# Optimization experiments

Hardware: AMD Instinct MI355X
Metric: run time of the kernel (lower is better)

## Reference

```python
import jax, jax.numpy as jnp
import numpy as np

K_TOP = 2  # n_experts_per_tok
W_SCALE = 0.02  # keep activations numerically tame


def setup_inputs() -> dict:
    key = jax.random.key(0)
    ks = jax.random.split(key, 8)
    D, F, E = 1024, 1024, 8
    B, T = 4, 2048
    x = jax.random.normal(ks[0], (B, T, D), dtype=jnp.float32)
    router_w = jax.random.normal(ks[1], (D, E), dtype=jnp.float32) * W_SCALE
    sg = jax.random.normal(ks[2], (D, F), dtype=jnp.float32) * W_SCALE
    su = jax.random.normal(ks[3], (D, F), dtype=jnp.float32) * W_SCALE
    sd = jax.random.normal(ks[4], (F, D), dtype=jnp.float32) * W_SCALE
    wg = jax.random.normal(ks[5], (E, D, F), dtype=jnp.float32) * W_SCALE
    wu = jax.random.normal(ks[6], (E, D, F), dtype=jnp.float32) * W_SCALE
    wd = jax.random.normal(ks[7], (E, F, D), dtype=jnp.float32) * W_SCALE
    return {"x": x, "router_w": router_w, "sg": sg, "su": su, "sd": sd,
            "wg": wg, "wu": wu, "wd": wd}


def reference(x, router_w, sg, su, sd, wg, wu, wd):
    B, T, D = x.shape
    E = wg.shape[0]
    flat = x.reshape(-1, D)                       # [N, D]
    N = flat.shape[0]

    # shared SwiGLU expert (n_shared_experts = 1)
    shared = (jax.nn.silu(flat @ sg) * (flat @ su)) @ sd  # [N, D]

    # top-k softmax router with renormalization
    probs = jax.nn.softmax(flat @ router_w, axis=-1)      # [N, E]
    topk_p, topk_i = jax.lax.top_k(probs, K_TOP)          # [N, K]
    topk_p = topk_p / (jnp.sum(topk_p, axis=-1, keepdims=True) + 1e-9)

    # dense combine weights: scatter renormalized probs into [N, E]
    cw = jnp.zeros((N, E), dtype=flat.dtype).at[
        jnp.arange(N)[:, None], topk_i].add(topk_p)

    # per-expert SwiGLU on all tokens, weighted combine (jit-friendly MoE form)
    h = jax.nn.silu(jnp.einsum('nd,edf->nef', flat, wg)) \
        * jnp.einsum('nd,edf->nef', flat, wu)             # [N, E, F]
    eo = jnp.einsum('nef,efd->ned', h, wd)                # [N, E, D]
    routed = jnp.einsum('ned,ne->nd', eo, cw)             # [N, D]

    return (shared + routed).reshape(B, T, D)
```

## Files before the change

kernel.cpp:

```cpp
#include <hip/hip_runtime.h>

#define N_TOK    8192
#define D_DIM    1024
#define F_DIM    1024
#define NESH     9
#define MAX_RTD  18432
#define MAX_ROWS 26624
#define BM 256
#define NK 16

#define MO 16
#define MT 25

typedef float  f4    __attribute__((ext_vector_type(4)));
typedef float  f32x4 __attribute__((ext_vector_type(4)));
typedef short  s16x8 __attribute__((ext_vector_type(8)));
typedef unsigned short u16x8 __attribute__((ext_vector_type(8)));
typedef unsigned short u16x4 __attribute__((ext_vector_type(4)));

static __device__ __forceinline__ unsigned short f2bf(float f) {
    union { float f; unsigned u; } v; v.f = f;
    unsigned r = v.u + 0x7FFFu + ((v.u >> 16) & 1u);
    return (unsigned short)(r >> 16);
}
static __device__ __forceinline__ float bf2f(unsigned short u) {
    union { unsigned u; float f; } v; v.u = ((unsigned)u) << 16; return v.f;
}

#define GLDS(gp, lp) __builtin_amdgcn_global_load_lds( \
    (const __attribute__((address_space(1))) void*)(gp), \
    (__attribute__((address_space(3))) void*)(lp), 16, 0, 0)

__global__ __launch_bounds__(256) void k_transpose(
    const float* __restrict__ wg, const float* __restrict__ wu,
    const float* __restrict__ wd, const float* __restrict__ sg,
    const float* __restrict__ su, const float* __restrict__ sd,
    unsigned short* __restrict__ wgt, unsigned short* __restrict__ wut,
    unsigned short* __restrict__ wdt)
{
    int bx = blockIdx.x;
    int m = bx >> 8;
    int tile = bx & 255;
    int ty = tile >> 4, tx = tile & 15;
    int set = m / 9, e = m % 9;
    const float* src; unsigned short* dst;
    if (set == 0)      { src = (e < 8) ? wg + (size_t)e*1048576 : sg; dst = wgt + (size_t)e*1048576; }
    else if (set == 1) { src = (e < 8) ? wu + (size_t)e*1048576 : su; dst = wut + (size_t)e*1048576; }
    else               { src = (e < 8) ? wd + (size_t)e*1048576 : sd; dst = wdt + (size_t)e*1048576; }

    __shared__ unsigned short ts[64 * 67];
    int t = threadIdx.x;
    int rT0 = ty * 64, cT0 = tx * 64;
    #pragma unroll
    for (int i = 0; i < 4; i++) {
        int idx = t + i * 256;
        int a  = idx >> 4;
        int b4 = (idx & 15) * 4;
        f4 v = *(const f4*)(src + (size_t)(cT0 + a) * 1024 + rT0 + b4);
        ts[a * 67 + b4 + 0] = f2bf(v[0]);
        ts[a * 67 + b4 + 1] = f2bf(v[1]);
        ts[a * 67 + b4 + 2] = f2bf(v[2]);
        ts[a * 67 + b4 + 3] = f2bf(v[3]);
    }
    __syncthreads();
    #pragma unroll
    for (int i = 0; i < 2; i++) {
        int slot = t + i * 256;
        int r  = slot >> 3;
        int c8 = (slot & 7) * 8;
        u16x8 o;
        #pragma unroll
        for (int k = 0; k < 8; k++) o[k] = ts[(c8 + k) * 67 + r];
        *(u16x8*)&dst[(size_t)(rT0 + r) * 1024 + cT0 + c8] = o;
    }
}

__global__ __launch_bounds__(256) void k_router(
    const float* __restrict__ x, const float* __restrict__ rw,
    unsigned short* __restrict__ xb,
    int* __restrict__ tk_i, float* __restrict__ tk_w)
{
    int wid = threadIdx.x >> 6, lane = threadIdx.x & 63;
    int n = blockIdx.x * 4 + wid;
    const float* xr = x + (size_t)n * D_DIM;
    unsigned short* xbr = xb + (size_t)n * D_DIM;
    float acc[8] = {0,0,0,0,0,0,0,0};
    #pragma unroll
    for (int it = 0; it < 4; it++) {
        int d0 = it * 256 + lane * 4;
        f4 xv = *(const f4*)(xr + d0);
        #pragma unroll
        for (int j = 0; j < 4; j++) {
            f4 r0 = *(const f4*)(rw + (size_t)(d0 + j) * 8);
            f4 r1 = *(const f4*)(rw + (size_t)(d0 + j) * 8 + 4);
            acc[0] += xv[j]*r0[0]; acc[1] += xv[j]*r0[1]; acc[2] += xv[j]*r0[2]; acc[3] += xv[j]*r0[3];
            acc[4] += xv[j]*r1[0]; acc[5] += xv[j]*r1[1]; acc[6] += xv[j]*r1[2]; acc[7] += xv[j]*r1[3];
        }
        u16x4 o; o[0]=f2bf(xv[0]); o[1]=f2bf(xv[1]); o[2]=f2bf(xv[2]); o[3]=f2bf(xv[3]);
        *(u16x4*)&xbr[d0] = o;
    }
    #pragma unroll
    for (int e = 0; e < 8; e++)
        for (int off = 32; off; off >>= 1)
            acc[e] += __shfl_xor(acc[e], off, 64);
    if (lane == 0) {
        float mx = acc[0];
        for (int e = 1; e < 8; e++) mx = fmaxf(mx, acc[e]);
        float p[8], s = 0.f;
        for (int e = 0; e < 8; e++) { p[e] = expf(acc[e] - mx); s += p[e]; }
        int i0 = 0;
        for (int e = 1; e < 8; e++) if (p[e] > p[i0]) i0 = e;
        int i1 = (i0 == 0) ? 1 : 0;
        for (int e = 0; e < 8; e++) if (e != i0 && p[e] > p[i1]) i1 = e;
        float p0 = p[i0] / s, p1 = p[i1] / s;
        float rs = p0 + p1 + 1e-9f;
        tk_i[2*n] = i0;  tk_i[2*n+1] = i1;
        tk_w[2*n] = p0 / rs;  tk_w[2*n+1] = p1 / rs;
    }
}

__global__ __launch_bounds__(1024) void k_count_scatter(
    const int* __restrict__ tk_i, const float* __restrict__ tk_w,
    int* __restrict__ meta,
    int* __restrict__ row_token, int* __restrict__ row_expert,
    int* __restrict__ tok_pos)
{
    __shared__ int cnt[1024 * 9];
    __shared__ int tot[8];
    __shared__ int off[9];
    const int t = threadIdx.x;
    const int lane = t & 63;
    const int wid = t >> 6;

    #pragma unroll
    for (int e = 0; e < 8; e++) cnt[t * 9 + e] = 0;
    __syncthreads();

    #pragma unroll
    for (int j = 0; j < 8; j++) {
        int n = t * 8 + j;
        cnt[t * 9 + tk_i[2 * n]]++;
        cnt[t * 9 + tk_i[2 * n + 1]]++;
    }
    __syncthreads();

    if (wid < 8) {
        const int e = wid;
        int carry = 0;
        for (int c = 0; c < 16; c++) {
            int i = c * 64 + lane;
            int v = cnt[i * 9 + e];
            int s = v;
            #pragma unroll
            for (int d = 1; d < 64; d <<= 1) {
                int u = __shfl_up(s, d, 64);
                if (lane >= d) s += u;
            }
            cnt[i * 9 + e] = s - v + carry;
            carry += __shfl(s, 63, 64);
        }
        if (lane == 0) tot[e] = carry;
    }
    __syncthreads();

    if (t == 0) {
        int acc = 0;
        #pragma unroll
        for (int e = 0; e < 8; e++) {
            off[e] = acc;
            meta[MO + e] = acc;
            acc += ((tot[e] + 255) >> 8) << 8;
        }
        off[8] = acc;
        meta[MO + 8] = acc;
        meta[MT] = acc + N_TOK;
    }
    __syncthreads();

    #pragma unroll
    for (int j = 0; j < 8; j++) {
        int n = t * 8 + j;
        #pragma unroll
        for (int k = 0; k < 2; k++) {
            int e = tk_i[2 * n + k];
            int pos = off[e] + cnt[t * 9 + e];
            cnt[t * 9 + e] = cnt[t * 9 + e] + 1;
            row_token[pos] = n; row_expert[pos] = e;
            tok_pos[2 * n + k] = pos;
        }
        int ps = off[8] + n;
        row_token[ps] = n; row_expert[ps] = 8;
    }
    #pragma unroll
    for (int e = 0; e < 8; e++) {
        int start = off[e] + tot[e], end = off[e + 1];
        for (int i = start + t; i < end; i += 1024) row_token[i] = -1;
    }
}

__global__ __launch_bounds__(512, 2) void k_gemm1(
    const unsigned short* __restrict__ xb,
    const unsigned short* __restrict__ wgt,
    const unsigned short* __restrict__ wut,
    const int* __restrict__ row_token,
    const int* __restrict__ row_expert,
    const int* __restrict__ meta,
    unsigned short* __restrict__ h)
{
    const int total = meta[MT];
    const int orig = blockIdx.x;
    const int bid = (orig & 7) * 104 + (orig >> 3);
    const int rt = bid >> 3, ct = bid & 7;
    const int row0 = rt * BM;
    if (row0 >= total) return;
    const int e = row_expert[row0];

    __shared__ __align__(16) unsigned short sA[4 * 256 * 32];
    __shared__ __align__(16) unsigned short sBg[4 * 128 * 32];
    __shared__ __align__(16) unsigned short sBu[4 * 128 * 32];

    const int t = threadIdx.x;
    const int lane = t & 63;
    const int klane = lane >> 4;
    const int wid = t >> 6;
    const int wr = wid >> 2, wc = wid & 3;

    const unsigned short* aA[2];
    #pragma unroll
    for (int r = 0; r < 2; r++) {
        int slot = t + r * 512;
        int row = slot >> 2;
        int cg = (slot & 3) ^ ((row >> 1) & 3);
        int tok = row_token[row0 + row];
        if (tok < 0) tok = 0;
        aA[r] = xb + (size_t)tok * D_DIM + cg * 8;
    }
    const int brow = t >> 2;
    const int bcg = (t & 3) ^ ((brow >> 1) & 3);
    const unsigned short* bG = wgt + ((size_t)e * F_DIM + ct * 128 + brow) * D_DIM + bcg * 8;
    const unsigned short* bU = wut + ((size_t)e * F_DIM + ct * 128 + brow) * D_DIM + bcg * 8;

#define ST_A(sl, ko) do { \
    GLDS(aA[0] + (ko), &sA[(sl) * 8192 + t * 8]); \
    GLDS(aA[1] + (ko), &sA[(sl) * 8192 + (t + 512) * 8]); } while (0)
#define ST_G(sl, ko) GLDS(bG + (ko), &sBg[(sl) * 4096 + t * 8])
#define ST_U(sl, ko) GLDS(bU + (ko), &sBu[(sl) * 4096 + t * 8])

#define G1_PHASE(bb, ss, hh, STAGE_STMT, VM_STMT) do { \
    const unsigned short* pA = &sA[((bb)*2 + (ss)) * 8192]; \
    const unsigned short* pG = &sBg[((bb)*2 + (ss)) * 4096]; \
    const unsigned short* pU = &sBu[((bb)*2 + (ss)) * 4096]; \
    s16x8 a_[4], g_[2], q_[2]; \
    _Pragma("unroll") \
    for (int mi = 0; mi < 4; mi++) { \
        int row = wr * 128 + (hh) * 64 + mi * 16 + (lane & 15); \
        a_[mi] = *(const s16x8*)&pA[row * 32 + ((klane ^ ((row >> 1) & 3)) << 3)]; } \
    _Pragma("unroll") \
    for (int ni = 0; ni < 2; ni++) { \
        int row = wc * 32 + ni * 16 + (lane & 15); \
        int ix = row * 32 + ((klane ^ ((row >> 1) & 3)) << 3); \
        g_[ni] = *(const s16x8*)&pG[ix]; \
        q_[ni] = *(const s16x8*)&pU[ix]; } \
    STAGE_STMT; \
    VM_STMT; \
    asm volatile("s_barrier" ::: "memory"); \
    __builtin_amdgcn_s_setprio(1); \
    _Pragma("unroll") \
    for (int mi = 0; mi < 4; mi++) \
        _Pragma("unroll") \
        for (int ni = 0; ni < 2; ni++) { \
            accg[(hh)*4+mi][ni] = __builtin_amdgcn_mfma_f32_16x16x32_bf16(a_[mi], g_[ni], accg[(hh)*4+mi][ni], 0, 0, 0); \
            accu[(hh)*4+mi][ni] = __builtin_amdgcn_mfma_f32_16x16x32_bf16(a_[mi], q_[ni], accu[(hh)*4+mi][ni], 0, 0, 0); } \
    __builtin_amdgcn_s_setprio(0); \
    asm volatile("s_barrier" ::: "memory"); \
} while (0)

    f32x4 accg[8][2] = {}, accu[8][2] = {};

    ST_A(0, 0);  ST_G(0, 0);  ST_U(0, 0);
    ST_A(1, 32); ST_G(1, 32); ST_U(1, 32);
    ST_A(2, 64); ST_G(2, 64); ST_U(2, 64);
    ST_A(3, 96);
    asm volatile("s_waitcnt vmcnt(6)" ::: "memory");
    asm volatile("s_barrier" ::: "memory");

    for (int u = 0; u < NK; u++) {
        const int b = u & 1, nb = b ^ 1;
        const int o1 = (u + 1) * 64 + 32, o2 = (u + 2) * 64;
        G1_PHASE(b, 0, 0, if (u < NK-1) { ST_G(nb*2+1, o1); ST_U(nb*2+1, o1); }, );
        G1_PHASE(b, 0, 1, if (u < NK-2) { ST_A(b*2, o2); }, );
        G1_PHASE(b, 1, 0, if (u < NK-2) { ST_G(b*2, o2); ST_U(b*2, o2); }, );
        G1_PHASE(b, 1, 1, if (u < NK-2) { ST_A(b*2+1, o2+32); },
                 if (u < NK-2) { asm volatile("s_waitcnt vmcnt(6)" ::: "memory"); }
                 else if (u == NK-2) { asm volatile("s_waitcnt vmcnt(0)" ::: "memory"); });
    }

    #pragma unroll
    for (int mf = 0; mf < 8; mf++)
        #pragma unroll
        for (int r = 0; r < 4; r++) {
            int grow = row0 + wr * 128 + mf * 16 + (lane >> 4) * 4 + r;
            unsigned short* hrow = h + (size_t)grow * F_DIM + ct * 128 + wc * 32 + (lane & 15);
            #pragma unroll
            for (int ni = 0; ni < 2; ni++) {
                float g = accg[mf][ni][r], uu = accu[mf][ni][r];
                float sv = g / (1.f + __expf(-g));
                hrow[ni * 16] = f2bf(sv * uu);
            }
        }
#undef ST_A
#undef ST_G
#undef ST_U
#undef G1_PHASE
}

__global__ __launch_bounds__(512, 2) void k_gemm2(
    const unsigned short* __restrict__ h,
    const unsigned short* __restrict__ wdt,
    const int* __restrict__ row_expert,
    const int* __restrict__ meta,
    unsigned short* __restrict__ eo,
    float* __restrict__ out)
{
    const int total = meta[MT];
    const int off8 = meta[MO + 8];
    const int orig = blockIdx.x;
    const int bid = (orig & 7) * 52 + (orig >> 3);
    const int rt = bid >> 2, ct = bid & 3;
    const int row0 = rt * BM;
    if (row0 >= total) return;
    const int e = row_expert[row0];

    __shared__ __align__(16) unsigned short sA[4 * 256 * 32];
    __shared__ __align__(16) unsigned short sB[4 * 256 * 32];

    const int t = threadIdx.x;
    const int lane = t & 63;
    const int klane = lane >> 4;
    const int wid = t >> 6;
    const int wr = wid >> 2, wc = wid & 3;

    const unsigned short* aA[2];
    const unsigned short* bB[2];
    #pragma unroll
    for (int r = 0; r < 2; r++) {
        int slot = t + r * 512;
        int row = slot >> 2;
        int cg = (slot & 3) ^ ((row >> 1) & 3);
        aA[r] = h + (size_t)(row0 + row) * F_DIM + cg * 8;
        bB[r] = wdt + ((size_t)e * D_DIM + ct * 256 + row) * F_DIM + cg * 8;
    }

#define ST_A2(sl, ko) do { \
    GLDS(aA[0] + (ko), &sA[(sl) * 8192 + t * 8]); \
    GLDS(aA[1] + (ko), &sA[(sl) * 8192 + (t + 512) * 8]); } while (0)
#define ST_B2(sl, ko) do { \
    GLDS(bB[0] + (ko), &sB[(sl) * 8192 + t * 8]); \
    GLDS(bB[1] + (ko), &sB[(sl) * 8192 + (t + 512) * 8]); } while (0)

#define G2_PHASE(bb, ss, hh, STAGE_STMT, VM_STMT) do { \
    const unsigned short* pA = &sA[((bb)*2 + (ss)) * 8192]; \
    const unsigned short* pB = &sB[((bb)*2 + (ss)) * 8192]; \
    s16x8 a_[4], b_[4]; \
    _Pragma("unroll") \
    for (int mi = 0; mi < 4; mi++) { \
        int row = wr * 128 + (hh) * 64 + mi * 16 + (lane & 15); \
        a_[mi] = *(const s16x8*)&pA[row * 32 + ((klane ^ ((row >> 1) & 3)) << 3)]; } \
    _Pragma("unroll") \
    for (int ni = 0; ni < 4; ni++) { \
        int row = wc * 64 + ni * 16 + (lane & 15); \
        b_[ni] = *(const s16x8*)&pB[row * 32 + ((klane ^ ((row >> 1) & 3)) << 3)]; } \
    STAGE_STMT; \
    VM_STMT; \
    asm volatile("s_barrier" ::: "memory"); \
    __builtin_amdgcn_s_setprio(1); \
    _Pragma("unroll") \
    for (int mi = 0; mi < 4; mi++) \
        _Pragma("unroll") \
        for (int ni = 0; ni < 4; ni++) \
            acc[(hh)*4+mi][ni] = __builtin_amdgcn_mfma_f32_16x16x32_bf16(a_[mi], b_[ni], acc[(hh)*4+mi][ni], 0, 0, 0); \
    __builtin_amdgcn_s_setprio(0); \
    asm volatile("s_barrier" ::: "memory"); \
} while (0)

    f32x4 acc[8][4] = {};

    ST_A2(0, 0);  ST_B2(0, 0);
    ST_A2(1, 32); ST_B2(1, 32);
    ST_A2(2, 64); ST_B2(2, 64);
    ST_A2(3, 96);
    asm volatile("s_waitcnt vmcnt(6)" ::: "memory");
    asm volatile("s_barrier" ::: "memory");

    for (int u = 0; u < NK; u++) {
        const int b = u & 1, nb = b ^ 1;
        const int o1 = (u + 1) * 64 + 32, o2 = (u + 2) * 64;
        G2_PHASE(b, 0, 0, if (u < NK-1) { ST_B2(nb*2+1, o1); }, );
        G2_PHASE(b, 0, 1, if (u < NK-2) { ST_A2(b*2, o2); }, );
        G2_PHASE(b, 1, 0, if (u < NK-2) { ST_B2(b*2, o2); }, );
        G2_PHASE(b, 1, 1, if (u < NK-2) { ST_A2(b*2+1, o2+32); },
                 if (u < NK-2) { asm volatile("s_waitcnt vmcnt(6)" ::: "memory"); }
                 else if (u == NK-2) { asm volatile("s_waitcnt vmcnt(0)" ::: "memory"); });
    }

    if (e < 8) {
        #pragma unroll
        for (int mf = 0; mf < 8; mf++)
            #pragma unroll
            for (int r = 0; r < 4; r++) {
                int grow = row0 + wr * 128 + mf * 16 + (lane >> 4) * 4 + r;
                unsigned short* erow = eo + (size_t)grow * D_DIM + ct * 256 + wc * 64 + (lane & 15);
                #pragma unroll
                for (int ni = 0; ni < 4; ni++)
                    erow[ni * 16] = f2bf(acc[mf][ni][r]);
            }
    } else {
        #pragma unroll
        for (int mf = 0; mf < 8; mf++)
            #pragma unroll
            for (int r = 0; r < 4; r++) {
                int grow = row0 + wr * 128 + mf * 16 + (lane >> 4) * 4 + r;
                int tok = grow - off8;
                float* orow = out + (size_t)tok * D_DIM + ct * 256 + wc * 64 + (lane & 15);
                #pragma unroll
                for (int ni = 0; ni < 4; ni++)
                    orow[ni * 16] = acc[mf][ni][r];
            }
    }
#undef ST_A2
#undef ST_B2
#undef G2_PHASE
}

__global__ __launch_bounds__(256) void k_combine(
    const unsigned short* __restrict__ eo,
    const int* __restrict__ tok_pos, const float* __restrict__ tk_w,
    float* __restrict__ out)
{
    const int t = threadIdx.x;
    const int n = blockIdx.x * 2 + (t >> 7);
    const int c0 = (t & 127) * 8;
    const int p0 = tok_pos[2 * n], p1 = tok_pos[2 * n + 1];
    const float w0 = tk_w[2 * n], w1 = tk_w[2 * n + 1];
    u16x8 a = *(const u16x8*)&eo[(size_t)p0 * D_DIM + c0];
    u16x8 b = *(const u16x8*)&eo[(size_t)p1 * D_DIM + c0];
    float* orow = out + (size_t)n * D_DIM + c0;
    f4 o0 = *(f4*)orow, o1 = *(f4*)(orow + 4);
    #pragma unroll
    for (int j = 0; j < 4; j++) {
        o0[j] += w0 * bf2f(a[j])     + w1 * bf2f(b[j]);
        o1[j] += w0 * bf2f(a[4 + j]) + w1 * bf2f(b[4 + j]);
    }
    *(f4*)orow = o0;
    *(f4*)(orow + 4) = o1;
}

extern "C" void kernel_launch(void* const* d_in, const int* in_sizes, int n_in,
                              void* d_out, int out_size, void* d_ws, size_t ws_size,
                              hipStream_t stream)
{
    const float* x  = (const float*)d_in[0];
    const float* rw = (const float*)d_in[1];
    const float* sg = (const float*)d_in[2];
    const float* su = (const float*)d_in[3];
    const float* sd = (const float*)d_in[4];
    const float* wg = (const float*)d_in[5];
    const float* wu = (const float*)d_in[6];
    const float* wd = (const float*)d_in[7];
    float* out = (float*)d_out;

    char* p = (char*)d_ws;
    unsigned short* xb  = (unsigned short*)p; p += (size_t)N_TOK * D_DIM * 2;
    unsigned short* wgt = (unsigned short*)p; p += (size_t)NESH * D_DIM * F_DIM * 2;
    unsigned short* wut = (unsigned short*)p; p += (size_t)NESH * D_DIM * F_DIM * 2;
    unsigned short* wdt = (unsigned short*)p; p += (size_t)NESH * D_DIM * F_DIM * 2;
    unsigned short* h   = (unsigned short*)p; p += (size_t)MAX_ROWS * F_DIM * 2;
    int*   row_token  = (int*)p;   p += (size_t)MAX_ROWS * 4;
    int*   row_expert = (int*)p;   p += (size_t)MAX_ROWS * 4;
    int*   tok_pos = (int*)p;      p += (size_t)N_TOK * 2 * 4;
    int*   tk_i = (int*)p;         p += (size_t)N_TOK * 2 * 4;
    float* tk_w = (float*)p;       p += (size_t)N_TOK * 2 * 4;
    int*   meta = (int*)p;         p += 1024;
    if ((size_t)(p - (char*)d_ws) > ws_size) return;

    unsigned short* eo = wgt;

    k_router<<<N_TOK / 4, 256, 0, stream>>>(x, rw, xb, tk_i, tk_w);
    k_transpose<<<27 * 256, 256, 0, stream>>>(wg, wu, wd, sg, su, sd, wgt, wut, wdt);
    k_count_scatter<<<1, 1024, 0, stream>>>(tk_i, tk_w, meta, row_token, row_expert, tok_pos);
    k_gemm1<<<(MAX_ROWS / BM) * 8, 512, 0, stream>>>(xb, wgt, wut, row_token, row_expert, meta, h);
    k_gemm2<<<(MAX_ROWS / BM) * 4, 512, 0, stream>>>(h, wdt, row_expert, meta, eo, out);
    k_combine<<<N_TOK / 2, 256, 0, stream>>>(eo, tok_pos, tk_w, out);
}
```

Measured before the change: 354.7 us.

## Restructure both GEMM pipelines to BK=64 double-buffered tiles with XOR-8 swizzle

Both grouped GEMM kernels move from four 32-wide K slots staged two iterations ahead to two 64-wide K buffers staged one iteration ahead. The LDS layout changes to 64-element rows with an 8-way XOR swizzle. B fragments are now held in registers across the two M-halves, so they are read from LDS once per K sub-step instead of twice. The cost is a shallower prefetch: each iteration ends on a full vmcnt(0) wait, which can expose global load latency.

After: 341.3 us. 3.8% less time.

```diff
diff --git a/kernel.cpp b/kernel.cpp
--- a/kernel.cpp
+++ b/kernel.cpp
@@ -7,6 +7,7 @@
 #define MAX_RTD  18432
 #define MAX_ROWS 26624
 #define BM 256
+#define BK 64
 #define NK 16
 
 #define MO 16
@@ -215,84 +216,96 @@
     if (row0 >= total) return;
     const int e = row_expert[row0];
 
-    __shared__ __align__(16) unsigned short sA[4 * 256 * 32];
-    __shared__ __align__(16) unsigned short sBg[4 * 128 * 32];
-    __shared__ __align__(16) unsigned short sBu[4 * 128 * 32];
+    __shared__ __align__(16) unsigned short sA[2 * 256 * 64];
+    __shared__ __align__(16) unsigned short sBg[2 * 128 * 64];
+    __shared__ __align__(16) unsigned short sBu[2 * 128 * 64];
 
     const int t = threadIdx.x;
     const int lane = t & 63;
-    const int klane = lane >> 4;
+    const int lr = lane & 15;
+    const int kl = lane >> 4;
     const int wid = t >> 6;
     const int wr = wid >> 2, wc = wid & 3;
 
-    const unsigned short* aA[2];
-    #pragma unroll
-    for (int r = 0; r < 2; r++) {
-        int slot = t + r * 512;
-        int row = slot >> 2;
-        int cg = (slot & 3) ^ ((row >> 1) & 3);
+    const unsigned short* asrc[4];
+    #pragma unroll
+    for (int i = 0; i < 4; i++) {
+        int slot = t + i * 512;
+        int row = slot >> 3;
+        int cg  = (slot & 7) ^ (row & 7);
         int tok = row_token[row0 + row];
         if (tok < 0) tok = 0;
-        aA[r] = xb + (size_t)tok * D_DIM + cg * 8;
-    }
-    const int brow = t >> 2;
-    const int bcg = (t & 3) ^ ((brow >> 1) & 3);
-    const unsigned short* bG = wgt + ((size_t)e * F_DIM + ct * 128 + brow) * D_DIM + bcg * 8;
-    const unsigned short* bU = wut + ((size_t)e * F_DIM + ct * 128 + brow) * D_DIM + bcg * 8;
-
-#define ST_A(sl, ko) do { \
-    GLDS(aA[0] + (ko), &sA[(sl) * 8192 + t * 8]); \
-    GLDS(aA[1] + (ko), &sA[(sl) * 8192 + (t + 512) * 8]); } while (0)
-#define ST_G(sl, ko) GLDS(bG + (ko), &sBg[(sl) * 4096 + t * 8])
-#define ST_U(sl, ko) GLDS(bU + (ko), &sBu[(sl) * 4096 + t * 8])
-
-#define G1_PHASE(bb, ss, hh, STAGE_STMT, VM_STMT) do { \
-    const unsigned short* pA = &sA[((bb)*2 + (ss)) * 8192]; \
-    const unsigned short* pG = &sBg[((bb)*2 + (ss)) * 4096]; \
-    const unsigned short* pU = &sBu[((bb)*2 + (ss)) * 4096]; \
-    s16x8 a_[4], g_[2], q_[2]; \
+        asrc[i] = xb + (size_t)tok * D_DIM + cg * 8;
+    }
+    const unsigned short* bsrcg[2];
+    const unsigned short* bsrcu[2];
+    #pragma unroll
+    for (int i = 0; i < 2; i++) {
+        int slot = t + i * 512;
+        int row = slot >> 3;
+        int cg  = (slot & 7) ^ (row & 7);
+        size_t off = ((size_t)e * F_DIM + ct * 128 + row) * D_DIM + cg * 8;
+        bsrcg[i] = wgt + off;
+        bsrcu[i] = wut + off;
+    }
+
+#define ST_A1(bb, k0) do { \
+    _Pragma("unroll") \
+    for (int i_ = 0; i_ < 4; i_++) \
+        GLDS(asrc[i_] + (k0), &sA[(bb) * 16384 + (t + i_ * 512) * 8]); \
+    } while (0)
+#define ST_B1(bb, k0) do { \
+    _Pragma("unroll") \
+    for (int i_ = 0; i_ < 2; i_++) { \
+        GLDS(bsrcg[i_] + (k0), &sBg[(bb) * 8192 + (t + i_ * 512) * 8]); \
+        GLDS(bsrcu[i_] + (k0), &sBu[(bb) * 8192 + (t + i_ * 512) * 8]); \
+    } } while (0)
+
+    f32x4 accg[8][2] = {}, accu[8][2] = {};
+    s16x8 a_[4], g_[2], u_[2];
+
+#define G1_PHASE(bb, mh, kk, RB, STG, VM) do { \
+    const unsigned short* pA = &sA[(bb) * 16384]; \
+    const unsigned short* pG = &sBg[(bb) * 8192]; \
+    const unsigned short* pU = &sBu[(bb) * 8192]; \
     _Pragma("unroll") \
     for (int mi = 0; mi < 4; mi++) { \
-        int row = wr * 128 + (hh) * 64 + mi * 16 + (lane & 15); \
-        a_[mi] = *(const s16x8*)&pA[row * 32 + ((klane ^ ((row >> 1) & 3)) << 3)]; } \
-    _Pragma("unroll") \
-    for (int ni = 0; ni < 2; ni++) { \
-        int row = wc * 32 + ni * 16 + (lane & 15); \
-        int ix = row * 32 + ((klane ^ ((row >> 1) & 3)) << 3); \
-        g_[ni] = *(const s16x8*)&pG[ix]; \
-        q_[ni] = *(const s16x8*)&pU[ix]; } \
-    STAGE_STMT; \
-    VM_STMT; \
-    asm volatile("s_barrier" ::: "memory"); \
+        int row = wr * 128 + (mh) * 64 + mi * 16 + lr; \
+        a_[mi] = *(const s16x8*)&pA[(row * 64 + (kk) * 32 + kl * 8) ^ ((row & 7) << 3)]; } \
+    if (RB) { \
+        _Pragma("unroll") \
+        for (int ni = 0; ni < 2; ni++) { \
+            int row = wc * 32 + ni * 16 + lr; \
+            int ix = (row * 64 + (kk) * 32 + kl * 8) ^ ((row & 7) << 3); \
+            g_[ni] = *(const s16x8*)&pG[ix]; \
+            u_[ni] = *(const s16x8*)&pU[ix]; } } \
+    STG; \
+    VM; \
+    __builtin_amdgcn_s_barrier(); \
     __builtin_amdgcn_s_setprio(1); \
     _Pragma("unroll") \
     for (int mi = 0; mi < 4; mi++) \
         _Pragma("unroll") \
         for (int ni = 0; ni < 2; ni++) { \
-            accg[(hh)*4+mi][ni] = __builtin_amdgcn_mfma_f32_16x16x32_bf16(a_[mi], g_[ni], accg[(hh)*4+mi][ni], 0, 0, 0); \
-            accu[(hh)*4+mi][ni] = __builtin_amdgcn_mfma_f32_16x16x32_bf16(a_[mi], q_[ni], accu[(hh)*4+mi][ni], 0, 0, 0); } \
+            accg[(mh)*4+mi][ni] = __builtin_amdgcn_mfma_f32_16x16x32_bf16(a_[mi], g_[ni], accg[(mh)*4+mi][ni], 0, 0, 0); \
+            accu[(mh)*4+mi][ni] = __builtin_amdgcn_mfma_f32_16x16x32_bf16(a_[mi], u_[ni], accu[(mh)*4+mi][ni], 0, 0, 0); } \
     __builtin_amdgcn_s_setprio(0); \
-    asm volatile("s_barrier" ::: "memory"); \
+    __builtin_amdgcn_s_barrier(); \
 } while (0)
 
-    f32x4 accg[8][2] = {}, accu[8][2] = {};
-
-    ST_A(0, 0);  ST_G(0, 0);  ST_U(0, 0);
-    ST_A(1, 32); ST_G(1, 32); ST_U(1, 32);
-    ST_A(2, 64); ST_G(2, 64); ST_U(2, 64);
-    ST_A(3, 96);
-    asm volatile("s_waitcnt vmcnt(6)" ::: "memory");
-    asm volatile("s_barrier" ::: "memory");
+    ST_A1(0, 0);
+    ST_B1(0, 0);
+    asm volatile("s_waitcnt vmcnt(0)" ::: "memory");
+    __builtin_amdgcn_s_barrier();
 
     for (int u = 0; u < NK; u++) {
         const int b = u & 1, nb = b ^ 1;
-        const int o1 = (u + 1) * 64 + 32, o2 = (u + 2) * 64;
-        G1_PHASE(b, 0, 0, if (u < NK-1) { ST_G(nb*2+1, o1); ST_U(nb*2+1, o1); }, );
-        G1_PHASE(b, 0, 1, if (u < NK-2) { ST_A(b*2, o2); }, );
-        G1_PHASE(b, 1, 0, if (u < NK-2) { ST_G(b*2, o2); ST_U(b*2, o2); }, );
-        G1_PHASE(b, 1, 1, if (u < NK-2) { ST_A(b*2+1, o2+32); },
-                 if (u < NK-2) { asm volatile("s_waitcnt vmcnt(6)" ::: "memory"); }
-                 else if (u == NK-2) { asm volatile("s_waitcnt vmcnt(0)" ::: "memory"); });
+        const int k1 = (u + 1) * BK;
+        G1_PHASE(b, 0, 0, 1, if (u < NK-1) ST_A1(nb, k1), );
+        G1_PHASE(b, 1, 0, 0, if (u < NK-1) ST_B1(nb, k1), );
+        G1_PHASE(b, 0, 1, 1, , );
+        G1_PHASE(b, 1, 1, 0, ,
+                 if (u < NK-1) { asm volatile("s_waitcnt vmcnt(0)" ::: "memory"); });
     }
 
     #pragma unroll
@@ -300,7 +313,7 @@
         #pragma unroll
         for (int r = 0; r < 4; r++) {
             int grow = row0 + wr * 128 + mf * 16 + (lane >> 4) * 4 + r;
-            unsigned short* hrow = h + (size_t)grow * F_DIM + ct * 128 + wc * 32 + (lane & 15);
+            unsigned short* hrow = h + (size_t)grow * F_DIM + ct * 128 + wc * 32 + lr;
             #pragma unroll
             for (int ni = 0; ni < 2; ni++) {
                 float g = accg[mf][ni][r], uu = accu[mf][ni][r];
@@ -308,9 +321,8 @@
                 hrow[ni * 16] = f2bf(sv * uu);
             }
         }
-#undef ST_A
-#undef ST_G
-#undef ST_U
+#undef ST_A1
+#undef ST_B1
 #undef G1_PHASE
 }
 
@@ -331,76 +343,79 @@
     if (row0 >= total) return;
     const int e = row_expert[row0];
 
-    __shared__ __align__(16) unsigned short sA[4 * 256 * 32];
-    __shared__ __align__(16) unsigned short sB[4 * 256 * 32];
+    __shared__ __align__(16) unsigned short sA[2 * 256 * 64];
+    __shared__ __align__(16) unsigned short sB[2 * 256 * 64];
 
     const int t = threadIdx.x;
     const int lane = t & 63;
-    const int klane = lane >> 4;
+    const int lr = lane & 15;
+    const int kl = lane >> 4;
     const int wid = t >> 6;
     const int wr = wid >> 2, wc = wid & 3;
 
-    const unsigned short* aA[2];
-    const unsigned short* bB[2];
-    #pragma unroll
-    for (int r = 0; r < 2; r++) {
-        int slot = t + r * 512;
-        int row = slot >> 2;
-        int cg = (slot & 3) ^ ((row >> 1) & 3);
-        aA[r] = h + (size_t)(row0 + row) * F_DIM + cg * 8;
-        bB[r] = wdt + ((size_t)e * D_DIM + ct * 256 + row) * F_DIM + cg * 8;
-    }
-
-#define ST_A2(sl, ko) do { \
-    GLDS(aA[0] + (ko), &sA[(sl) * 8192 + t * 8]); \
-    GLDS(aA[1] + (ko), &sA[(sl) * 8192 + (t + 512) * 8]); } while (0)
-#define ST_B2(sl, ko) do { \
-    GLDS(bB[0] + (ko), &sB[(sl) * 8192 + t * 8]); \
-    GLDS(bB[1] + (ko), &sB[(sl) * 8192 + (t + 512) * 8]); } while (0)
-
-#define G2_PHASE(bb, ss, hh, STAGE_STMT, VM_STMT) do { \
-    const unsigned short* pA = &sA[((bb)*2 + (ss)) * 8192]; \
-    const unsigned short* pB = &sB[((bb)*2 + (ss)) * 8192]; \
-    s16x8 a_[4], b_[4]; \
+    const unsigned short* asrc[4];
+    const unsigned short* bsrc[4];
+    #pragma unroll
+    for (int i = 0; i < 4; i++) {
+        int slot = t + i * 512;
+        int row = slot >> 3;
+        int cg  = (slot & 7) ^ (row & 7);
+        asrc[i] = h + (size_t)(row0 + row) * F_DIM + cg * 8;
+        bsrc[i] = wdt + ((size_t)e * D_DIM + ct * 256 + row) * F_DIM + cg * 8;
+    }
+
+#define ST_A2(bb, k0) do { \
+    _Pragma("unroll") \
+    for (int i_ = 0; i_ < 4; i_++) \
+        GLDS(asrc[i_] + (k0), &sA[(bb) * 16384 + (t + i_ * 512) * 8]); \
+    } while (0)
+#define ST_B2(bb, k0) do { \
+    _Pragma("unroll") \
+    for (int i_ = 0; i_ < 4; i_++) \
+        GLDS(bsrc[i_] + (k0), &sB[(bb) * 16384 + (t + i_ * 512) * 8]); \
+    } while (0)
+
+    f32x4 acc[8][4] = {};
+    s16x8 a_[4], b_[4];
+
+#define G2_PHASE(bb, mh, kk, RB, STG, VM) do { \
+    const unsigned short* pA = &sA[(bb) * 16384]; \
+    const unsigned short* pB = &sB[(bb) * 16384]; \
     _Pragma("unroll") \
     for (int mi = 0; mi < 4; mi++) { \
-        int row = wr * 128 + (hh) * 64 + mi * 16 + (lane & 15); \
-        a_[mi] = *(const s16x8*)&pA[row * 32 + ((klane ^ ((row >> 1) & 3)) << 3)]; } \
-    _Pragma("unroll") \
-    for (int ni = 0; ni < 4; ni++) { \
-        int row = wc * 64 + ni * 16 + (lane & 15); \
-        b_[ni] = *(const s16x8*)&pB[row * 32 + ((klane ^ ((row >> 1) & 3)) << 3)]; } \
-    STAGE_STMT; \
-    VM_STMT; \
-    asm volatile("s_barrier" ::: "memory"); \
+        int row = wr * 128 + (mh) * 64 + mi * 16 + lr; \
+        a_[mi] = *(const s16x8*)&pA[(row * 64 + (kk) * 32 + kl * 8) ^ ((row & 7) << 3)]; } \
+    if (RB) { \
+        _Pragma("unroll") \
+        for (int ni = 0; ni < 4; ni++) { \
+            int row = wc * 64 + ni * 16 + lr; \
+            b_[ni] = *(const s16x8*)&pB[(row * 64 + (kk) * 32 + kl * 8) ^ ((row & 7) << 3)]; } } \
+    STG; \
+    VM; \
+    __builtin_amdgcn_s_barrier(); \
     __builtin_amdgcn_s_setprio(1); \
     _Pragma("unroll") \
     for (int mi = 0; mi < 4; mi++) \
         _Pragma("unroll") \
         for (int ni = 0; ni < 4; ni++) \
-            acc[(hh)*4+mi][ni] = __builtin_amdgcn_mfma_f32_16x16x32_bf16(a_[mi], b_[ni], acc[(hh)*4+mi][ni], 0, 0, 0); \
+            acc[(mh)*4+mi][ni] = __builtin_amdgcn_mfma_f32_16x16x32_bf16(a_[mi], b_[ni], acc[(mh)*4+mi][ni], 0, 0, 0); \
     __builtin_amdgcn_s_setprio(0); \
-    asm volatile("s_barrier" ::: "memory"); \
+    __builtin_amdgcn_s_barrier(); \
 } while (0)
 
-    f32x4 acc[8][4] = {};
-
-    ST_A2(0, 0);  ST_B2(0, 0);
-    ST_A2(1, 32); ST_B2(1, 32);
-    ST_A2(2, 64); ST_B2(2, 64);
-    ST_A2(3, 96);
-    asm volatile("s_waitcnt vmcnt(6)" ::: "memory");
-    asm volatile("s_barrier" ::: "memory");
+    ST_A2(0, 0);
+    ST_B2(0, 0);
+    asm volatile("s_waitcnt vmcnt(0)" ::: "memory");
+    __builtin_amdgcn_s_barrier();
 
     for (int u = 0; u < NK; u++) {
         const int b = u & 1, nb = b ^ 1;
-        const int o1 = (u + 1) * 64 + 32, o2 = (u + 2) * 64;
-        G2_PHASE(b, 0, 0, if (u < NK-1) { ST_B2(nb*2+1, o1); }, );
-        G2_PHASE(b, 0, 1, if (u < NK-2) { ST_A2(b*2, o2); }, );
-        G2_PHASE(b, 1, 0, if (u < NK-2) { ST_B2(b*2, o2); }, );
-        G2_PHASE(b, 1, 1, if (u < NK-2) { ST_A2(b*2+1, o2+32); },
-                 if (u < NK-2) { asm volatile("s_waitcnt vmcnt(6)" ::: "memory"); }
-                 else if (u == NK-2) { asm volatile("s_waitcnt vmcnt(0)" ::: "memory"); });
+        const int k1 = (u + 1) * BK;
+        G2_PHASE(b, 0, 0, 1, if (u < NK-1) ST_A2(nb, k1), );
+        G2_PHASE(b, 1, 0, 0, if (u < NK-1) ST_B2(nb, k1), );
+        G2_PHASE(b, 0, 1, 1, , );
+        G2_PHASE(b, 1, 1, 0, ,
+                 if (u < NK-1) { asm volatile("s_waitcnt vmcnt(0)" ::: "memory"); });
     }
 
     if (e < 8) {
@@ -409,7 +424,7 @@
             #pragma unroll
             for (int r = 0; r < 4; r++) {
                 int grow = row0 + wr * 128 + mf * 16 + (lane >> 4) * 4 + r;
-                unsigned short* erow = eo + (size_t)grow * D_DIM + ct * 256 + wc * 64 + (lane & 15);
+                unsigned short* erow = eo + (size_t)grow * D_DIM + ct * 256 + wc * 64 + lr;
                 #pragma unroll
                 for (int ni = 0; ni < 4; ni++)
                     erow[ni * 16] = f2bf(acc[mf][ni][r]);
@@ -421,7 +436,7 @@
             for (int r = 0; r < 4; r++) {
                 int grow = row0 + wr * 128 + mf * 16 + (lane >> 4) * 4 + r;
                 int tok = grow - off8;
-                float* orow = out + (size_t)tok * D_DIM + ct * 256 + wc * 64 + (lane & 15);
+                float* orow = out + (size_t)tok * D_DIM + ct * 256 + wc * 64 + lr;
                 #pragma unroll
                 for (int ni = 0; ni < 4; ni++)
                     orow[ni * 16] = acc[mf][ni][r];
```
